# Performance work log

Measured on AMD Instinct MI355X. Metric: run time of the kernel, lower is better.

Reference implementation:

```python
import jax, jax.numpy as jnp
import numpy as np

DIM = 768
D_STATE = 16
D_INNER = 2 * DIM  # expand=2


def setup_inputs() -> dict:
    key = jax.random.key(0)
    k_x, k_in, k_conv, k_out = jax.random.split(key, 4)
    B, L = 1, 4096
    x = jax.random.normal(k_x, (B, L, DIM), dtype=jnp.float32)
    # torch Linear weight layout: [out_features, in_features]
    W_in = jax.random.normal(k_in, (3 * D_INNER + 2 * D_STATE, DIM), dtype=jnp.float32) * 0.02
    # depthwise conv1d kernel: [out_ch=d_inner, in_ch/groups=1, k=3]
    W_conv = jax.random.normal(k_conv, (D_INNER, 1, 3), dtype=jnp.float32) * 0.1
    W_out = jax.random.normal(k_out, (DIM, D_INNER), dtype=jnp.float32) * 0.02
    A_log = jnp.log(jnp.tile(jnp.arange(1, D_STATE + 1, dtype=jnp.float32), (D_INNER, 1)))
    D = jnp.ones((D_INNER,), dtype=jnp.float32)
    return {"x": x, "W_in": W_in, "W_conv": W_conv, "W_out": W_out, "A_log": A_log, "D": D}


def reference(x, W_in, W_conv, W_out, A_log, D):
    d_inner = W_conv.shape[0]
    d_state = A_log.shape[1]
    Bsz = x.shape[0]

    xz = x @ W_in.T  # [B, L, 3*d_inner + 2*d_state]
    x_inner, z, B_ssm, C_ssm, delta = jnp.split(
        xz, [d_inner, 2 * d_inner, 2 * d_inner + d_state, 2 * d_inner + 2 * d_state], axis=-1
    )

    # depthwise conv over sequence: [B, d_inner, L]
    xc = jax.lax.conv_general_dilated(
        x_inner.transpose(0, 2, 1), W_conv,
        window_strides=(1,), padding=[(1, 1)], feature_group_count=d_inner,
    ).transpose(0, 2, 1)  # back to [B, L, d_inner]
    xc = jax.nn.silu(xc)

    A = -jnp.exp(A_log)  # [d_inner, d_state]
    delta = jax.nn.softplus(delta)  # [B, L, d_inner]
    dA = jnp.exp(jnp.einsum('bld,dn->bldn', delta, A))           # [B, L, d_inner, d_state]
    dBx = jnp.einsum('bld,bln,bld->bldn', delta, B_ssm, xc)      # delta_B * x fused

    def step(h, inp):
        da_t, dbx_t, c_t = inp  # [B,d,n], [B,d,n], [B,n]
        h = da_t * h + dbx_t
        y_t = jnp.einsum('bdn,bn->bd', h, c_t)
        return h, y_t

    h0 = jnp.zeros((Bsz, d_inner, d_state), dtype=x.dtype)
    _, ys = jax.lax.scan(
        step, h0,
        (dA.transpose(1, 0, 2, 3), dBx.transpose(1, 0, 2, 3), C_ssm.transpose(1, 0, 2)),
    )  # ys: [L, B, d_inner]

    y = ys.transpose(1, 0, 2) + xc * D  # skip connection
    y = y * jax.nn.silu(z)
    return y @ W_out.T  # [B, L, dim]
```

## Files before the change

### kernel.cpp

```cpp
#include <hip/hip_runtime.h>
#include <hip/hip_bf16.h>
#include <math.h>

#define LSEQ   4096
#define DIM    768
#define DINNER 1536
#define DSTATE 16
#define NCOLS  4640
#define NCH    128
#define CLEN   32
#define NPAD   4736
#define DXW    1568

typedef _Float16 f16;
typedef __attribute__((ext_vector_type(8))) _Float16 f16x8;
typedef __attribute__((ext_vector_type(4))) float f32x4;

__device__ __forceinline__ void gld_lds16(void* lds_dst, const void* gsrc) {
    __builtin_amdgcn_global_load_lds(
        (__attribute__((address_space(1))) void*)(gsrc),
        (__attribute__((address_space(3))) void*)(lds_dst), 16, 0, 0);
}

template<int BM, int BN, int WM, int WN, int NTB, bool COLM, bool ZMODE>
__global__ __launch_bounds__(256) void gemm_f16(const f16* __restrict__ A,
                                                const f16* __restrict__ B,
                                                float* __restrict__ C,
                                                f16* __restrict__ Xb,
                                                f16* __restrict__ Zb,
                                                int M, int N, int K, int ldc) {
    constexpr int MI  = WM / 16;
    constexpr int NI  = WN / 16;
    constexpr int NWN = BN / WN;
    constexpr int RT  = BM + BN;
    constexpr int NS  = RT / 8;

    __shared__ __align__(16) f16 S[RT * 64];
    f16* As = S;
    f16* Bs = S + BM * 64;

    const int P   = gridDim.x >> 3;
    const int idx = (blockIdx.x & 7) * P + (blockIdx.x >> 3);
    const int m0  = (COLM ? (idx % NTB) : (idx / NTB)) * BM;
    const int n0  = (COLM ? (idx / NTB) : (idx % NTB)) * BN;

    const int tid  = threadIdx.x;
    const int w    = tid >> 6;
    const int lane = tid & 63;
    const int wr   = w / NWN;
    const int wc   = w % NWN;
    const int m    = lane & 15;
    const int q    = lane >> 4;
    const int rl8  = lane >> 3;
    const int bsel = lane & 7;

    f32x4 acc[MI][NI];
#pragma unroll
    for (int i = 0; i < MI; i++)
#pragma unroll
        for (int j = 0; j < NI; j++) acc[i][j] = (f32x4){0.f, 0.f, 0.f, 0.f};

    for (int k0 = 0; k0 < K; k0 += 64) {
#pragma unroll
        for (int t = w; t < NS; t += 4) {
            const int rl  = t * 8 + rl8;
            const int blk = bsel ^ (rl & 7);
            const f16* g = (rl < BM)
                ? A + (size_t)(m0 + rl) * K + k0 + blk * 8
                : B + (size_t)(n0 + rl - BM) * K + k0 + blk * 8;
            gld_lds16(S + t * 8 * 64, g);
        }
        __syncthreads();

#pragma unroll
        for (int kk = 0; kk < 2; kk++) {
            const int fo = (((q + 4 * kk) ^ (m & 7)) << 3);
            f16x8 af[MI], bh[NI];
#pragma unroll
            for (int i = 0; i < MI; i++)
                af[i] = *(const f16x8*)&As[(wr * WM + i * 16 + m) * 64 + fo];
#pragma unroll
            for (int j = 0; j < NI; j++)
                bh[j] = *(const f16x8*)&Bs[(wc * WN + j * 16 + m) * 64 + fo];
#pragma unroll
            for (int i = 0; i < MI; i++)
#pragma unroll
                for (int j = 0; j < NI; j++)
                    acc[i][j] = __builtin_amdgcn_mfma_f32_16x16x32_f16(
                        af[i], bh[j], acc[i][j], 0, 0, 0);
        }
        __syncthreads();
    }

    if (ZMODE && n0 < DINNER) {
#pragma unroll
        for (int i = 0; i < MI; i++)
#pragma unroll
            for (int j = 0; j < NI; j++) {
                const int col  = n0 + wc * WN + j * 16 + m;
                const int rowb = m0 + wr * WM + i * 16 + q * 4;
#pragma unroll
                for (int r = 0; r < 4; r++)
                    Xb[(size_t)(rowb + r) * DINNER + col] = (f16)acc[i][j][r];
            }
        return;
    }
    if (ZMODE && n0 < 2 * DINNER) {
#pragma unroll
        for (int i = 0; i < MI; i++)
#pragma unroll
            for (int j = 0; j < NI; j++) {
                const int col  = n0 - DINNER + wc * WN + j * 16 + m;
                const int rowb = m0 + wr * WM + i * 16 + q * 4;
#pragma unroll
                for (int r = 0; r < 4; r++)
                    Zb[(size_t)(rowb + r) * DINNER + col] = (f16)acc[i][j][r];
            }
        return;
    }
#pragma unroll
    for (int i = 0; i < MI; i++)
#pragma unroll
        for (int j = 0; j < NI; j++) {
            const int col  = (ZMODE ? n0 - 2 * DINNER : n0) + wc * WN + j * 16 + m;
            const int lim  = ZMODE ? DXW : N;
            if (col >= lim) continue;
            const int rowb = m0 + wr * WM + i * 16 + q * 4;
#pragma unroll
            for (int r = 0; r < 4; r++)
                C[(size_t)(rowb + r) * ldc + col] = acc[i][j][r];
        }
}

#define E0 (LSEQ * DIM)
#define E1 (E0 + NPAD * DIM)
#define E2 (E1 + DIM * DINNER)

__global__ __launch_bounds__(256) void cvt_all(const float* __restrict__ x,
                                               const float* __restrict__ Wi,
                                               const float* __restrict__ Wo,
                                               f16* __restrict__ Ax,
                                               f16* __restrict__ Bw,
                                               f16* __restrict__ Bo) {
    int i = (blockIdx.x * 256 + threadIdx.x) * 4;
    if (i < E0) {
        float4 v = *(const float4*)(x + i);
        Ax[i] = (f16)v.x; Ax[i+1] = (f16)v.y; Ax[i+2] = (f16)v.z; Ax[i+3] = (f16)v.w;
    } else if (i < E1) {
        int e = i - E0;
        int n = e / DIM;
        if (n < NCOLS) {
            float4 v = *(const float4*)(Wi + e);
            Bw[e] = (f16)v.x; Bw[e+1] = (f16)v.y; Bw[e+2] = (f16)v.z; Bw[e+3] = (f16)v.w;
        } else {
            Bw[e] = (f16)0.f; Bw[e+1] = (f16)0.f; Bw[e+2] = (f16)0.f; Bw[e+3] = (f16)0.f;
        }
    } else if (i < E2) {
        int e = i - E1;
        float4 v = *(const float4*)(Wo + e);
        Bo[e] = (f16)v.x; Bo[e+1] = (f16)v.y; Bo[e+2] = (f16)v.z; Bo[e+3] = (f16)v.w;
    }
}

__global__ __launch_bounds__(256) void scan1_kernel(const float* __restrict__ Dxz,
                                                    const f16* __restrict__ Xb,
                                                    const float* __restrict__ Wc,
                                                    const float* __restrict__ A_log,
                                                    float* __restrict__ aprod,
                                                    float* __restrict__ hend) {
    __shared__ float Bs[CLEN * DSTATE];
    const int d  = blockIdx.x * 256 + threadIdx.x;
    const int c  = blockIdx.y;
    const int l0 = c * CLEN;
    for (int i = threadIdx.x; i < CLEN * DSTATE; i += 256)
        Bs[i] = Dxz[(size_t)(l0 + (i >> 4)) * DXW + (i & 15)];
    float Areg[DSTATE];
#pragma unroll
    for (int n = 0; n < DSTATE; n++) Areg[n] = -__expf(A_log[d * DSTATE + n]);
    const float w0 = Wc[d * 3 + 0], w1 = Wc[d * 3 + 1], w2 = Wc[d * 3 + 2];
    float xm = (l0 > 0) ? (float)Xb[(size_t)(l0 - 1) * DINNER + d] : 0.f;
    float x0 = (float)Xb[(size_t)l0 * DINNER + d];
    float ld_xp   = (float)Xb[(size_t)(l0 + 1) * DINNER + d];
    float ld_draw = Dxz[(size_t)l0 * DXW + 32 + d];
    __syncthreads();

    float h[DSTATE];
#pragma unroll
    for (int n = 0; n < DSTATE; n++) h[n] = 0.f;
    float S = 0.f;

    for (int t = 0; t < CLEN; t++) {
        const int l = l0 + t;
        float xp = ld_xp, draw = ld_draw;
        if (t + 1 < CLEN) {
            ld_xp   = (l + 2 < LSEQ) ? (float)Xb[(size_t)(l + 2) * DINNER + d] : 0.f;
            ld_draw = Dxz[(size_t)(l + 1) * DXW + 32 + d];
        }
        float v  = xm * w0 + x0 * w1 + xp * w2;
        float xcv = __fdividef(v, 1.f + __expf(-v));
        float dtv = (draw > 20.f) ? draw : __logf(1.f + __expf(draw));
        float u = dtv * xcv;
        S += dtv;
#pragma unroll
        for (int n = 0; n < DSTATE; n++) {
            float e = __expf(dtv * Areg[n]);
            h[n] = e * h[n] + u * Bs[t * DSTATE + n];
        }
        xm = x0; x0 = xp;
    }
#pragma unroll
    for (int n = 0; n < DSTATE; n++) {
        size_t idx = ((size_t)c * DSTATE + n) * DINNER + d;
        aprod[idx] = __expf(S * Areg[n]);
        hend[idx]  = h[n];
    }
}

__global__ __launch_bounds__(256) void scan2_kernel(const float* __restrict__ aprod,
                                                    const float* __restrict__ hend,
                                                    float* __restrict__ hinit) {
    const int g = blockIdx.x * 256 + threadIdx.x;
    const size_t S = (size_t)DSTATE * DINNER;
    size_t idx = g;
    float a = aprod[idx], e = hend[idx];
    float h = 0.f;
#pragma unroll 4
    for (int c = 0; c < NCH; c++) {
        float ac = a, ec = e;
        if (c + 1 < NCH) { a = aprod[idx + S]; e = hend[idx + S]; }
        hinit[idx] = h;
        h = ac * h + ec;
        idx += S;
    }
}

__global__ __launch_bounds__(256) void scan3_kernel(const float* __restrict__ Dxz,
                                                    const f16* __restrict__ Xb,
                                                    const f16* __restrict__ Zb,
                                                    const float* __restrict__ Wc,
                                                    const float* __restrict__ A_log,
                                                    const float* __restrict__ hinit,
                                                    const float* __restrict__ Dp,
                                                    f16* __restrict__ Ay) {
    __shared__ float Bs[CLEN * DSTATE];
    __shared__ float Cs[CLEN * DSTATE];
    const int d  = blockIdx.x * 256 + threadIdx.x;
    const int c  = blockIdx.y;
    const int l0 = c * CLEN;
    for (int i = threadIdx.x; i < CLEN * DSTATE; i += 256) {
        size_t roff = (size_t)(l0 + (i >> 4)) * DXW;
        Bs[i] = Dxz[roff + (i & 15)];
        Cs[i] = Dxz[roff + 16 + (i & 15)];
    }
    float Areg[DSTATE];
#pragma unroll
    for (int n = 0; n < DSTATE; n++) Areg[n] = -__expf(A_log[d * DSTATE + n]);
    float h[DSTATE];
#pragma unroll
    for (int n = 0; n < DSTATE; n++)
        h[n] = hinit[((size_t)c * DSTATE + n) * DINNER + d];
    const float Dv = Dp[d];
    const float w0 = Wc[d * 3 + 0], w1 = Wc[d * 3 + 1], w2 = Wc[d * 3 + 2];
    float xm = (l0 > 0) ? (float)Xb[(size_t)(l0 - 1) * DINNER + d] : 0.f;
    float x0 = (float)Xb[(size_t)l0 * DINNER + d];
    float ld_xp   = (float)Xb[(size_t)(l0 + 1) * DINNER + d];
    float ld_draw = Dxz[(size_t)l0 * DXW + 32 + d];
    float ld_z    = (float)Zb[(size_t)l0 * DINNER + d];
    __syncthreads();

    for (int t = 0; t < CLEN; t++) {
        const int l = l0 + t;
        float xp = ld_xp, draw = ld_draw, zv = ld_z;
        if (t + 1 < CLEN) {
            ld_xp   = (l + 2 < LSEQ) ? (float)Xb[(size_t)(l + 2) * DINNER + d] : 0.f;
            ld_draw = Dxz[(size_t)(l + 1) * DXW + 32 + d];
            ld_z    = (float)Zb[(size_t)(l + 1) * DINNER + d];
        }
        float v  = xm * w0 + x0 * w1 + xp * w2;
        float xcv = __fdividef(v, 1.f + __expf(-v));
        float dtv = (draw > 20.f) ? draw : __logf(1.f + __expf(draw));
        float u = dtv * xcv;
        float y = 0.f;
#pragma unroll
        for (int n = 0; n < DSTATE; n++) {
            float e = __expf(dtv * Areg[n]);
            h[n] = e * h[n] + u * Bs[t * DSTATE + n];
            y += h[n] * Cs[t * DSTATE + n];
        }
        float sz = __fdividef(zv, 1.f + __expf(-zv));
        Ay[(size_t)l * DINNER + d] = (f16)((y + xcv * Dv) * sz);
        xm = x0; x0 = xp;
    }
}

extern "C" void kernel_launch(void* const* d_in, const int* in_sizes, int n_in,
                              void* d_out, int out_size, void* d_ws, size_t ws_size,
                              hipStream_t stream) {
    const float* x     = (const float*)d_in[0];
    const float* W_in  = (const float*)d_in[1];
    const float* W_conv= (const float*)d_in[2];
    const float* W_out = (const float*)d_in[3];
    const float* A_log = (const float*)d_in[4];
    const float* Dp    = (const float*)d_in[5];
    float* out = (float*)d_out;

    float* ws  = (float*)d_ws;
    float* Dxz = ws;
    float* ap  = Dxz + (size_t)LSEQ * DXW;
    float* he  = ap + (size_t)NCH * DSTATE * DINNER;
    float* hi  = he + (size_t)NCH * DSTATE * DINNER;
    f16* Ax = (f16*)(hi + (size_t)NCH * DSTATE * DINNER);
    f16* Ay = Ax + (size_t)LSEQ * DIM;
    f16* Bw = Ay + (size_t)LSEQ * DINNER;
    f16* Bo = Bw + (size_t)NPAD * DIM;
    f16* Zb = Bo + (size_t)DIM * DINNER;
    f16* Xb = Zb + (size_t)LSEQ * DINNER;

    cvt_all<<<E2 / 1024, 256, 0, stream>>>(x, W_in, W_out, Ax, Bw, Bo);

    gemm_f16<128, 128, 64, 64, 32, true, true><<<1184, 256, 0, stream>>>(
        Ax, Bw, Dxz, Xb, Zb, LSEQ, NCOLS, DIM, DXW);

    scan1_kernel<<<dim3(DINNER / 256, NCH), 256, 0, stream>>>(
        Dxz, Xb, W_conv, A_log, ap, he);
    scan2_kernel<<<(DINNER * DSTATE) / 256, 256, 0, stream>>>(ap, he, hi);
    scan3_kernel<<<dim3(DINNER / 256, NCH), 256, 0, stream>>>(
        Dxz, Xb, Zb, W_conv, A_log, hi, Dp, Ay);

    gemm_f16<64, 64, 32, 32, 12, false, false><<<768, 256, 0, stream>>>(
        Ay, Bo, out, nullptr, nullptr, LSEQ, DIM, DINNER, DIM);
}
```

Measured before the change: 246.6 us.

## Double-buffer GEMM K-loop and split delta/BC output into compact buffers

```diff
diff --git a/kernel.cpp b/kernel.cpp
--- a/kernel.cpp
+++ b/kernel.cpp
@@ -10,7 +10,6 @@
 #define NCH    128
 #define CLEN   32
 #define NPAD   4736
-#define DXW    1568
 
 typedef _Float16 f16;
 typedef __attribute__((ext_vector_type(8))) _Float16 f16x8;
@@ -28,16 +27,17 @@
                                                 float* __restrict__ C,
                                                 f16* __restrict__ Xb,
                                                 f16* __restrict__ Zb,
+                                                float* __restrict__ BC,
+                                                f16* __restrict__ Db,
                                                 int M, int N, int K, int ldc) {
     constexpr int MI  = WM / 16;
     constexpr int NI  = WN / 16;
     constexpr int NWN = BN / WN;
     constexpr int RT  = BM + BN;
-    constexpr int NS  = RT / 8;
-
-    __shared__ __align__(16) f16 S[RT * 64];
-    f16* As = S;
-    f16* Bs = S + BM * 64;
+    constexpr int NS  = RT / 16;
+    constexpr int SSZ = RT * 32;
+
+    __shared__ __align__(16) f16 S[2 * SSZ];
 
     const int P   = gridDim.x >> 3;
     const int idx = (blockIdx.x & 7) * P + (blockIdx.x >> 3);
@@ -51,8 +51,10 @@
     const int wc   = w % NWN;
     const int m    = lane & 15;
     const int q    = lane >> 4;
-    const int rl8  = lane >> 3;
-    const int bsel = lane & 7;
+    const int ell  = lane >> 3;
+    const int b8   = (lane & 7) ^ ell;
+    const int rofs = 2 * ell + (b8 >> 2);
+    const int kofs = (b8 & 3) * 8;
 
     f32x4 acc[MI][NI];
 #pragma unroll
@@ -60,35 +62,45 @@
 #pragma unroll
         for (int j = 0; j < NI; j++) acc[i][j] = (f32x4){0.f, 0.f, 0.f, 0.f};
 
-    for (int k0 = 0; k0 < K; k0 += 64) {
+    auto stage = [&](int st, int k0) {
 #pragma unroll
         for (int t = w; t < NS; t += 4) {
-            const int rl  = t * 8 + rl8;
-            const int blk = bsel ^ (rl & 7);
-            const f16* g = (rl < BM)
-                ? A + (size_t)(m0 + rl) * K + k0 + blk * 8
-                : B + (size_t)(n0 + rl - BM) * K + k0 + blk * 8;
-            gld_lds16(S + t * 8 * 64, g);
-        }
-        __syncthreads();
-
-#pragma unroll
-        for (int kk = 0; kk < 2; kk++) {
-            const int fo = (((q + 4 * kk) ^ (m & 7)) << 3);
-            f16x8 af[MI], bh[NI];
-#pragma unroll
-            for (int i = 0; i < MI; i++)
-                af[i] = *(const f16x8*)&As[(wr * WM + i * 16 + m) * 64 + fo];
+            const int rl = t * 16 + rofs;
+            const f16* g = (t * 16 < BM)
+                ? A + (size_t)(m0 + rl) * K + k0 + kofs
+                : B + (size_t)(n0 + rl - BM) * K + k0 + kofs;
+            gld_lds16(S + st * SSZ + t * 512, g);
+        }
+    };
+
+    const int NK = K / 32;
+    stage(0, 0);
+    __syncthreads();
+
+    for (int s = 0; s < NK; s++) {
+        if (s + 1 < NK) stage((s + 1) & 1, (s + 1) * 32);
+        const f16* sb = S + (s & 1) * SSZ;
+        f16x8 af[MI], bh[NI];
+#pragma unroll
+        for (int i = 0; i < MI; i++) {
+            const int R = wr * WM + i * 16 + m;
+            const int line = R >> 1;
+            const int slot = ((((R & 1) << 2) | q) ^ (line & 7));
+            af[i] = *(const f16x8*)&sb[line * 64 + slot * 8];
+        }
+#pragma unroll
+        for (int j = 0; j < NI; j++) {
+            const int R = BM + wc * WN + j * 16 + m;
+            const int line = R >> 1;
+            const int slot = ((((R & 1) << 2) | q) ^ (line & 7));
+            bh[j] = *(const f16x8*)&sb[line * 64 + slot * 8];
+        }
+#pragma unroll
+        for (int i = 0; i < MI; i++)
 #pragma unroll
             for (int j = 0; j < NI; j++)
-                bh[j] = *(const f16x8*)&Bs[(wc * WN + j * 16 + m) * 64 + fo];
-#pragma unroll
-            for (int i = 0; i < MI; i++)
-#pragma unroll
-                for (int j = 0; j < NI; j++)
-                    acc[i][j] = __builtin_amdgcn_mfma_f32_16x16x32_f16(
-                        af[i], bh[j], acc[i][j], 0, 0, 0);
-        }
+                acc[i][j] = __builtin_amdgcn_mfma_f32_16x16x32_f16(
+                    af[i], bh[j], acc[i][j], 0, 0, 0);
         __syncthreads();
     }
 
@@ -118,13 +130,31 @@
             }
         return;
     }
+    if (ZMODE) {
+#pragma unroll
+        for (int i = 0; i < MI; i++)
+#pragma unroll
+            for (int j = 0; j < NI; j++) {
+                const int col  = n0 + wc * WN + j * 16 + m;
+                const int rowb = m0 + wr * WM + i * 16 + q * 4;
+                if (col < 3104) {
+#pragma unroll
+                    for (int r = 0; r < 4; r++)
+                        BC[(size_t)(rowb + r) * 32 + (col - 3072)] = acc[i][j][r];
+                } else if (col < NCOLS) {
+#pragma unroll
+                    for (int r = 0; r < 4; r++)
+                        Db[(size_t)(rowb + r) * DINNER + (col - 3104)] = (f16)acc[i][j][r];
+                }
+            }
+        return;
+    }
 #pragma unroll
     for (int i = 0; i < MI; i++)
 #pragma unroll
         for (int j = 0; j < NI; j++) {
-            const int col  = (ZMODE ? n0 - 2 * DINNER : n0) + wc * WN + j * 16 + m;
-            const int lim  = ZMODE ? DXW : N;
-            if (col >= lim) continue;
+            const int col  = n0 + wc * WN + j * 16 + m;
+            if (col >= N) continue;
             const int rowb = m0 + wr * WM + i * 16 + q * 4;
 #pragma unroll
             for (int r = 0; r < 4; r++)
@@ -162,8 +192,9 @@
     }
 }
 
-__global__ __launch_bounds__(256) void scan1_kernel(const float* __restrict__ Dxz,
+__global__ __launch_bounds__(256) void scan1_kernel(const float* __restrict__ BC,
                                                     const f16* __restrict__ Xb,
+                                                    const f16* __restrict__ Db,
                                                     const float* __restrict__ Wc,
                                                     const float* __restrict__ A_log,
                                                     float* __restrict__ aprod,
@@ -173,7 +204,7 @@
     const int c  = blockIdx.y;
     const int l0 = c * CLEN;
     for (int i = threadIdx.x; i < CLEN * DSTATE; i += 256)
-        Bs[i] = Dxz[(size_t)(l0 + (i >> 4)) * DXW + (i & 15)];
+        Bs[i] = BC[(size_t)(l0 + (i >> 4)) * 32 + (i & 15)];
     float Areg[DSTATE];
 #pragma unroll
     for (int n = 0; n < DSTATE; n++) Areg[n] = -__expf(A_log[d * DSTATE + n]);
@@ -181,7 +212,7 @@
     float xm = (l0 > 0) ? (float)Xb[(size_t)(l0 - 1) * DINNER + d] : 0.f;
     float x0 = (float)Xb[(size_t)l0 * DINNER + d];
     float ld_xp   = (float)Xb[(size_t)(l0 + 1) * DINNER + d];
-    float ld_draw = Dxz[(size_t)l0 * DXW + 32 + d];
+    float ld_draw = (float)Db[(size_t)l0 * DINNER + d];
     __syncthreads();
 
     float h[DSTATE];
@@ -194,7 +225,7 @@
         float xp = ld_xp, draw = ld_draw;
         if (t + 1 < CLEN) {
             ld_xp   = (l + 2 < LSEQ) ? (float)Xb[(size_t)(l + 2) * DINNER + d] : 0.f;
-            ld_draw = Dxz[(size_t)(l + 1) * DXW + 32 + d];
+            ld_draw = (float)Db[(size_t)(l + 1) * DINNER + d];
         }
         float v  = xm * w0 + x0 * w1 + xp * w2;
         float xcv = __fdividef(v, 1.f + __expf(-v));
@@ -234,8 +265,9 @@
     }
 }
 
-__global__ __launch_bounds__(256) void scan3_kernel(const float* __restrict__ Dxz,
+__global__ __launch_bounds__(256) void scan3_kernel(const float* __restrict__ BC,
                                                     const f16* __restrict__ Xb,
+                                                    const f16* __restrict__ Db,
                                                     const f16* __restrict__ Zb,
                                                     const float* __restrict__ Wc,
                                                     const float* __restrict__ A_log,
@@ -248,9 +280,9 @@
     const int c  = blockIdx.y;
     const int l0 = c * CLEN;
     for (int i = threadIdx.x; i < CLEN * DSTATE; i += 256) {
-        size_t roff = (size_t)(l0 + (i >> 4)) * DXW;
-        Bs[i] = Dxz[roff + (i & 15)];
-        Cs[i] = Dxz[roff + 16 + (i & 15)];
+        size_t roff = (size_t)(l0 + (i >> 4)) * 32;
+        Bs[i] = BC[roff + (i & 15)];
+        Cs[i] = BC[roff + 16 + (i & 15)];
     }
     float Areg[DSTATE];
 #pragma unroll
@@ -264,7 +296,7 @@
     float xm = (l0 > 0) ? (float)Xb[(size_t)(l0 - 1) * DINNER + d] : 0.f;
     float x0 = (float)Xb[(size_t)l0 * DINNER + d];
     float ld_xp   = (float)Xb[(size_t)(l0 + 1) * DINNER + d];
-    float ld_draw = Dxz[(size_t)l0 * DXW + 32 + d];
+    float ld_draw = (float)Db[(size_t)l0 * DINNER + d];
     float ld_z    = (float)Zb[(size_t)l0 * DINNER + d];
     __syncthreads();
 
@@ -273,7 +305,7 @@
         float xp = ld_xp, draw = ld_draw, zv = ld_z;
         if (t + 1 < CLEN) {
             ld_xp   = (l + 2 < LSEQ) ? (float)Xb[(size_t)(l + 2) * DINNER + d] : 0.f;
-            ld_draw = Dxz[(size_t)(l + 1) * DXW + 32 + d];
+            ld_draw = (float)Db[(size_t)(l + 1) * DINNER + d];
             ld_z    = (float)Zb[(size_t)(l + 1) * DINNER + d];
         }
         float v  = xm * w0 + x0 * w1 + xp * w2;
@@ -305,8 +337,8 @@
     float* out = (float*)d_out;
 
     float* ws  = (float*)d_ws;
-    float* Dxz = ws;
-    float* ap  = Dxz + (size_t)LSEQ * DXW;
+    float* BC  = ws;
+    float* ap  = BC + (size_t)LSEQ * 32;
     float* he  = ap + (size_t)NCH * DSTATE * DINNER;
     float* hi  = he + (size_t)NCH * DSTATE * DINNER;
     f16* Ax = (f16*)(hi + (size_t)NCH * DSTATE * DINNER);
@@ -315,18 +347,19 @@
     f16* Bo = Bw + (size_t)NPAD * DIM;
     f16* Zb = Bo + (size_t)DIM * DINNER;
     f16* Xb = Zb + (size_t)LSEQ * DINNER;
+    f16* Db = Xb + (size_t)LSEQ * DINNER;
 
     cvt_all<<<E2 / 1024, 256, 0, stream>>>(x, W_in, W_out, Ax, Bw, Bo);
 
     gemm_f16<128, 128, 64, 64, 32, true, true><<<1184, 256, 0, stream>>>(
-        Ax, Bw, Dxz, Xb, Zb, LSEQ, NCOLS, DIM, DXW);
+        Ax, Bw, nullptr, Xb, Zb, BC, Db, LSEQ, NCOLS, DIM, 0);
 
     scan1_kernel<<<dim3(DINNER / 256, NCH), 256, 0, stream>>>(
-        Dxz, Xb, W_conv, A_log, ap, he);
+        BC, Xb, Db, W_conv, A_log, ap, he);
     scan2_kernel<<<(DINNER * DSTATE) / 256, 256, 0, stream>>>(ap, he, hi);
     scan3_kernel<<<dim3(DINNER / 256, NCH), 256, 0, stream>>>(
-        Dxz, Xb, Zb, W_conv, A_log, hi, Dp, Ay);
+        BC, Xb, Db, Zb, W_conv, A_log, hi, Dp, Ay);
 
     gemm_f16<64, 64, 32, 32, 12, false, false><<<768, 256, 0, stream>>>(
-        Ay, Bo, out, nullptr, nullptr, LSEQ, DIM, DINNER, DIM);
-}
+        Ay, Bo, out, nullptr, nullptr, nullptr, nullptr, LSEQ, DIM, DINNER, DIM);
+}
```

Measured after the change: 247.9 us. Within noise of the previous version (+0.5%).
